# Optimization experiments

Hardware: AMD Instinct MI355X
Metric: run time of the kernel (lower is better)

Reference implementation:

```python
import jax, jax.numpy as jnp
import numpy as np

NUM_LAYERS = 4
HIDDEN = 512
HEADS = 8
DK = HIDDEN // HEADS
REPR_IN = 53
REPR_HID = 32
LN_EPS = 1e-5


def _mask_by_1dmask(x, mask):
    # x: [B,H,L,L], mask: [B,L] bool
    pair = mask[:, :, None] & mask[:, None, :]          # [B,L,L]
    masked = jnp.where(pair[:, None, :, :], x, -jnp.inf)
    all_inf = jnp.all(masked == -jnp.inf, axis=-1, keepdims=True)
    return jnp.where(all_inf, 0.0, masked)


def _layernorm(x, g, b):
    mu = jnp.mean(x, axis=-1, keepdims=True)
    var = jnp.mean((x - mu) ** 2, axis=-1, keepdims=True)
    return (x - mu) * jax.lax.rsqrt(var + LN_EPS) * g + b


def _attn_block(x, mask, refCov, Wq, bq, Wk, bk, Wv, bv, Wo, bo,
                Wr1, br1, Wr2, br2, ln_g, ln_b):
    B, L, h = x.shape
    residual = x
    q = (x @ Wq + bq).reshape(B, L, HEADS, DK).transpose(0, 2, 1, 3)  # [B,H,L,dk]
    k = (x @ Wk + bk).reshape(B, L, HEADS, DK).transpose(0, 2, 1, 3)
    v = (x @ Wv + bv).reshape(B, L, HEADS, DK).transpose(0, 2, 1, 3)
    scores = jnp.einsum('bhid,bhjd->bhij', q, k) / np.sqrt(DK).astype(np.float32)
    scores = _mask_by_1dmask(scores, mask)
    attn_w = jax.nn.softmax(scores, axis=-1)
    # per-pair MLP bias: [B,L,L,53] -> [B,L,L,H] -> [B,H,L,L]
    ref = jax.nn.relu(refCov @ Wr1 + br1) @ Wr2 + br2
    ref = ref.transpose(0, 3, 1, 2)
    ref = _mask_by_1dmask(ref, mask)
    ref_w = jax.nn.softmax(ref, axis=-1)
    comb = attn_w + ref_w
    comb = comb / jnp.sum(comb, axis=-1, keepdims=True)
    out = jnp.einsum('bhij,bhjd->bhid', comb, v)
    out = out.transpose(0, 2, 1, 3).reshape(B, L, h)
    out = out @ Wo + bo
    return _layernorm(residual + out, ln_g, ln_b)


def setup_inputs() -> dict:
    key = jax.random.key(0)
    ks = jax.random.split(key, 20)
    B, L = 8, 384
    s = 0.02
    inp = {
        'x': jax.random.normal(ks[0], (B, L, HIDDEN), jnp.float32),
        'mask': jax.random.randint(ks[1], (B, L), 0, 2) > 0,
        'refCov': jax.random.normal(ks[2], (B, L, L, REPR_IN), jnp.float32),
        'Wq': jax.random.normal(ks[3], (NUM_LAYERS, HIDDEN, HIDDEN)) * s,
        'bq': jnp.zeros((NUM_LAYERS, HIDDEN)),
        'Wk': jax.random.normal(ks[4], (NUM_LAYERS, HIDDEN, HIDDEN)) * s,
        'bk': jnp.zeros((NUM_LAYERS, HIDDEN)),
        'Wv': jax.random.normal(ks[5], (NUM_LAYERS, HIDDEN, HIDDEN)) * s,
        'bv': jnp.zeros((NUM_LAYERS, HIDDEN)),
        'Wo': jax.random.normal(ks[6], (NUM_LAYERS, HIDDEN, HIDDEN)) * s,
        'bo': jnp.zeros((NUM_LAYERS, HIDDEN)),
        'Wr1': jax.random.normal(ks[7], (NUM_LAYERS, REPR_IN, REPR_HID)) * 0.1,
        'br1': jnp.zeros((NUM_LAYERS, REPR_HID)),
        'Wr2': jax.random.normal(ks[8], (NUM_LAYERS, REPR_HID, HEADS)) * 0.1,
        'br2': jnp.zeros((NUM_LAYERS, HEADS)),
        'ln_g': jnp.ones((NUM_LAYERS, HIDDEN)),
        'ln_b': jnp.zeros((NUM_LAYERS, HIDDEN)),
        'fn_g': jnp.ones((HIDDEN,)),
        'fn_b': jnp.zeros((HIDDEN,)),
    }
    return inp


def reference(x, mask, refCov, Wq, bq, Wk, bk, Wv, bv, Wo, bo,
              Wr1, br1, Wr2, br2, ln_g, ln_b, fn_g, fn_b):
    # process_node_feature packs flat nodes into [B,L,h] with zeros at padding;
    # equivalent here to zeroing padded positions of x.
    h = x * mask[:, :, None].astype(x.dtype)
    for i in range(NUM_LAYERS):
        h = _attn_block(h, mask, refCov, Wq[i], bq[i], Wk[i], bk[i],
                        Wv[i], bv[i], Wo[i], bo[i], Wr1[i], br1[i],
                        Wr2[i], br2[i], ln_g[i], ln_b[i])
    h = _layernorm(h, fn_g, fn_b)
    return jnp.sum(h * mask[:, :, None].astype(h.dtype), axis=1)  # [B, HIDDEN]
```

## Files before the change

kernel.cpp:

```cpp
#include <hip/hip_runtime.h>
#include <hip/hip_bf16.h>
#include <cstdint>

constexpr int LSEQ  = 384;
constexpr int BATCH = 8;
constexpr int HID   = 512;
constexpr int NHEAD = 8;
constexpr int DKH   = 64;
constexpr int NLAY  = 4;
constexpr int BL    = BATCH * LSEQ;
constexpr int LL2   = LSEQ * LSEQ;
constexpr int BH    = BATCH * NHEAD;

typedef __bf16 bf16x8 __attribute__((ext_vector_type(8)));
typedef float  f32x4  __attribute__((ext_vector_type(4)));
typedef unsigned short ushort_t;

__device__ inline bf16x8 load_frag(const void* p) {
    uint4 u = *reinterpret_cast<const uint4*>(p);
    return __builtin_bit_cast(bf16x8, u);
}
__device__ inline bf16x8 zero_frag() {
    uint4 u = {0u, 0u, 0u, 0u};
    return __builtin_bit_cast(bf16x8, u);
}
__device__ inline f32x4 mfma16(bf16x8 a, bf16x8 b, f32x4 c) {
    return __builtin_amdgcn_mfma_f32_16x16x32_bf16(a, b, c, 0, 0, 0);
}
__device__ inline float b2f(__hip_bfloat16 v) { return __bfloat162float(v); }
__device__ inline ushort_t bfbits(float f) {
    __hip_bfloat16 b = __float2bfloat16(f);
    return *(ushort_t*)&b;
}

__global__ __launch_bounds__(1024) void mask_norm_kernel(
    const unsigned char* __restrict__ raw, unsigned char* __restrict__ m)
{
    __shared__ int fl;
    const int tid = threadIdx.x;
    if (tid == 0) fl = 0;
    __syncthreads();
    int f = 0;
    for (int i = tid; i < BL; i += 1024) {
        const unsigned char v = raw[i];
        if (v > 1) f |= 1;
        if (v && (i & 3)) f |= 2;
        if (v && ((i & 7) == 4)) f |= 4;
        if (v && ((i & 3) <= 1)) f |= 8;
    }
    if (f) atomicOr(&fl, f);
    __syncthreads();
    const int ff = fl;
    int stride, off;
    if (ff & 1) { if (ff & 8) { stride = 2; off = 0; } else { stride = 4; off = 2; } }
    else if (ff & 2) { stride = 1; off = 0; }
    else if (ff & 4) { stride = 4; off = 0; }
    else             { stride = 8; off = 0; }
    for (int i = tid; i < BL; i += 1024)
        m[i] = raw[(size_t)i * stride + off] ? 1 : 0;
}

__global__ __launch_bounds__(256) void wconv_kernel(
    const float* __restrict__ Wq, const float* __restrict__ Wk,
    const float* __restrict__ Wv, const float* __restrict__ Wo,
    ushort_t* __restrict__ WTqkv, ushort_t* __restrict__ WTo)
{
    __shared__ float tile[32][33];
    const int t = blockIdx.x;
    const int ml = t >> 8;
    const int rest = t & 255;
    const int mi = ml >> 2, l = ml & 3;
    const int tk = (rest & 15) * 32;
    const int tn = (rest >> 4) * 32;
    const float* W = (mi == 0) ? Wq : (mi == 1) ? Wk : (mi == 2) ? Wv : Wo;
    const float* src = W + (size_t)l * HID * HID;
    const int c = threadIdx.x & 31, r = threadIdx.x >> 5;
    for (int rr = r; rr < 32; rr += 8)
        tile[rr][c] = src[(size_t)(tk + rr) * HID + tn + c];
    __syncthreads();
    ushort_t* dst = (mi < 3)
        ? WTqkv + ((size_t)l * 1536 + mi * 512) * HID
        : WTo   + (size_t)l * HID * HID;
    for (int rr = r; rr < 32; rr += 8)
        dst[(size_t)(tn + rr) * HID + tk + c] = bfbits(tile[c][rr]);
}

__global__ __launch_bounds__(256) void refw_kernel(
    const float* __restrict__ Wr1, const float* __restrict__ Wr2,
    ushort_t* __restrict__ W1T, ushort_t* __restrict__ W2T)
{
    const int tid = blockIdx.x * 256 + threadIdx.x;
    if (tid < 4 * 32 * 64) {
        const int l = tid >> 11, rem = tid & 2047;
        const int n = rem >> 6, k = rem & 63;
        W1T[tid] = (k < 53) ? bfbits(Wr1[(l * 53 + k) * 32 + n]) : (ushort_t)0;
    } else if (tid < 4 * 32 * 64 + 4 * 16 * 32) {
        const int t2 = tid - 8192;
        const int l = t2 >> 9, rem = t2 & 511;
        const int n = rem >> 5, k = rem & 31;
        W2T[t2] = (n < 8) ? bfbits(Wr2[(l * 32 + k) * 8 + n]) : (ushort_t)0;
    }
}

__global__ __launch_bounds__(256) void pack_kernel(
    const float* __restrict__ x, const unsigned char* __restrict__ mask,
    float* __restrict__ h, __hip_bfloat16* __restrict__ hb)
{
    const int idx = blockIdx.x * 256 + threadIdx.x;
    const int row = idx >> 9;
    const float v = mask[row] ? x[idx] : 0.f;
    h[idx] = v;
    hb[idx] = __float2bfloat16(v);
}

__global__ __launch_bounds__(256) void refmlp_kernel(
    const float* __restrict__ refCov,
    const ushort_t* __restrict__ W1T, const float* __restrict__ br1,
    const ushort_t* __restrict__ W2T, const float* __restrict__ br2,
    __hip_bfloat16* __restrict__ refL)
{
    __shared__ ushort_t smem[256 * 56];

    const int tid = threadIdx.x;
    const int w = tid >> 6, lane = tid & 63;
    const int lr = lane & 15, quad = lane >> 4;
    const size_t p0 = (size_t)blockIdx.x * 256;
    const int b = (int)(p0 / LL2);
    const int rem0 = (int)(p0 - (size_t)b * LL2);

    const float4* src4 = reinterpret_cast<const float4*>(refCov + p0 * 53);
    for (int f = tid; f < 3392; f += 256) {
        float4 v = src4[f];
        const int e = f * 4;
        #pragma unroll
        for (int k = 0; k < 4; ++k) {
            const int g = e + k;
            const int row = g / 53;
            const int col = g - row * 53;
            smem[row * 56 + col] = bfbits(((const float*)&v)[k]);
        }
    }
    smem[tid * 56 + 53] = 0;
    smem[tid * 56 + 54] = 0;
    smem[tid * 56 + 55] = 0;
    __syncthreads();

    bf16x8 afr[4][2];
    #pragma unroll
    for (int mi = 0; mi < 4; ++mi) {
        const ushort_t* rp = smem + (w * 64 + mi * 16 + lr) * 56;
        afr[mi][0] = load_frag(rp + quad * 8);
        afr[mi][1] = (quad < 3) ? load_frag(rp + 32 + quad * 8) : zero_frag();
    }
    __syncthreads();

    ushort_t* C1w = smem + w * 2560;

    #pragma unroll
    for (int l = 0; l < NLAY; ++l) {
        const float bias0 = br1[l * 32 + lr];
        const float bias1 = br1[l * 32 + 16 + lr];
        const float bias2 = br2[l * 8 + (lr & 7)];
        bf16x8 w1f[2][2];
        #pragma unroll
        for (int ni = 0; ni < 2; ++ni)
            #pragma unroll
            for (int ks = 0; ks < 2; ++ks)
                w1f[ni][ks] = load_frag(W1T + ((l * 32 + ni * 16 + lr) * 64) + ks * 32 + quad * 8);
        bf16x8 w2f = load_frag(W2T + (l * 16 + lr) * 32 + quad * 8);

        f32x4 acc[4][2];
        #pragma unroll
        for (int mi = 0; mi < 4; ++mi) {
            acc[mi][0] = (f32x4){bias0, bias0, bias0, bias0};
            acc[mi][1] = (f32x4){bias1, bias1, bias1, bias1};
        }
        #pragma unroll
        for (int mi = 0; mi < 4; ++mi) {
            acc[mi][0] = mfma16(afr[mi][0], w1f[0][0], acc[mi][0]);
            acc[mi][0] = mfma16(afr[mi][1], w1f[0][1], acc[mi][0]);
            acc[mi][1] = mfma16(afr[mi][0], w1f[1][0], acc[mi][1]);
            acc[mi][1] = mfma16(afr[mi][1], w1f[1][1], acc[mi][1]);
        }
        #pragma unroll
        for (int mi = 0; mi < 4; ++mi)
            #pragma unroll
            for (int ni = 0; ni < 2; ++ni)
                #pragma unroll
                for (int r = 0; r < 4; ++r)
                    C1w[(mi * 16 + quad * 4 + r) * 40 + ni * 16 + lr] =
                        bfbits(fmaxf(acc[mi][ni][r], 0.f));

        #pragma unroll
        for (int mi = 0; mi < 4; ++mi) {
            bf16x8 a2 = load_frag(C1w + (mi * 16 + lr) * 40 + quad * 8);
            f32x4 a = (f32x4){bias2, bias2, bias2, bias2};
            a = mfma16(a2, w2f, a);
            if (lr < 8) {
                uint2 pk;
                pk.x = (unsigned)bfbits(a[0]) | ((unsigned)bfbits(a[1]) << 16);
                pk.y = (unsigned)bfbits(a[2]) | ((unsigned)bfbits(a[3]) << 16);
                const size_t plane = ((size_t)(l * 8 + b) * 8 + lr) * LL2;
                *reinterpret_cast<uint2*>((ushort_t*)refL + plane + rem0 +
                                          w * 64 + mi * 16 + quad * 4) = pk;
            }
        }
    }
}

__global__ __launch_bounds__(256) void gemm_qkv_kernel(
    const __hip_bfloat16* __restrict__ A,
    const __hip_bfloat16* __restrict__ BT,
    const float* __restrict__ bq, const float* __restrict__ bk,
    const float* __restrict__ bv,
    __hip_bfloat16* __restrict__ q, __hip_bfloat16* __restrict__ kk,
    __hip_bfloat16* __restrict__ vT)
{
    const int bm = blockIdx.x % (BL / 64);
    const int bn = blockIdx.x / (BL / 64);
    const int wv = threadIdx.x >> 6;
    const int lane = threadIdx.x & 63;
    const int lr = lane & 15, quad = lane >> 4;
    const int m0 = bm * 64 + (wv & 1) * 32;
    const int n0g = bn * 64 + (wv >> 1) * 32;
    f32x4 acc[2][2];
    #pragma unroll
    for (int i = 0; i < 2; ++i)
        #pragma unroll
        for (int j = 0; j < 2; ++j) acc[i][j] = (f32x4){0.f, 0.f, 0.f, 0.f};
    const __hip_bfloat16* a0p = A + (size_t)(m0 + lr) * HID;
    const __hip_bfloat16* a1p = A + (size_t)(m0 + 16 + lr) * HID;
    const __hip_bfloat16* b0p = BT + (size_t)(n0g + lr) * HID;
    const __hip_bfloat16* b1p = BT + (size_t)(n0g + 16 + lr) * HID;
    #pragma unroll 4
    for (int k0 = 0; k0 < HID; k0 += 32) {
        const int ka = k0 + quad * 8;
        bf16x8 a0 = load_frag(a0p + ka);
        bf16x8 a1 = load_frag(a1p + ka);
        bf16x8 b0 = load_frag(b0p + ka);
        bf16x8 b1 = load_frag(b1p + ka);
        acc[0][0] = mfma16(a0, b0, acc[0][0]);
        acc[0][1] = mfma16(a0, b1, acc[0][1]);
        acc[1][0] = mfma16(a1, b0, acc[1][0]);
        acc[1][1] = mfma16(a1, b1, acc[1][1]);
    }
    const int mat = n0g >> 9;
    const float* bias = (mat == 0) ? bq : (mat == 1) ? bk : bv;
    const float scale = (mat == 0) ? 0.125f : 1.0f;
    __hip_bfloat16* outp = (mat == 0) ? q : (mat == 1) ? kk : vT;
    #pragma unroll
    for (int mi = 0; mi < 2; ++mi)
        #pragma unroll
        for (int ni = 0; ni < 2; ++ni)
            #pragma unroll
            for (int r = 0; r < 4; ++r) {
                const int m = m0 + mi * 16 + quad * 4 + r;
                const int ng = n0g + ni * 16 + lr;
                const int n = ng & 511;
                float v = (acc[mi][ni][r] + bias[n]) * scale;
                const int bb = m / LSEQ, ii = m % LSEQ;
                const int hh = n >> 6, d = n & 63;
                if (mat == 2)
                    outp[((size_t)(bb * NHEAD + hh) * DKH + d) * LSEQ + ii] = __float2bfloat16(v);
                else
                    outp[((size_t)(bb * NHEAD + hh) * LSEQ + ii) * DKH + d] = __float2bfloat16(v);
            }
}

__global__ __launch_bounds__(256) void gemm_oproj_kernel(
    const __hip_bfloat16* __restrict__ A,
    const __hip_bfloat16* __restrict__ BT,
    const float* __restrict__ bias,
    float* __restrict__ outf)
{
    const int bm = blockIdx.x % (BL / 64);
    const int bn = blockIdx.x / (BL / 64);
    const int wv = threadIdx.x >> 6;
    const int lane = threadIdx.x & 63;
    const int lr = lane & 15, quad = lane >> 4;
    const int m0 = bm * 64 + (wv & 1) * 32;
    const int n0 = bn * 64 + (wv >> 1) * 32;
    f32x4 acc[2][2];
    #pragma unroll
    for (int i = 0; i < 2; ++i)
        #pragma unroll
        for (int j = 0; j < 2; ++j) acc[i][j] = (f32x4){0.f, 0.f, 0.f, 0.f};
    const __hip_bfloat16* a0p = A + (size_t)(m0 + lr) * HID;
    const __hip_bfloat16* a1p = A + (size_t)(m0 + 16 + lr) * HID;
    const __hip_bfloat16* b0p = BT + (size_t)(n0 + lr) * HID;
    const __hip_bfloat16* b1p = BT + (size_t)(n0 + 16 + lr) * HID;
    #pragma unroll 4
    for (int k0 = 0; k0 < HID; k0 += 32) {
        const int ka = k0 + quad * 8;
        bf16x8 a0 = load_frag(a0p + ka);
        bf16x8 a1 = load_frag(a1p + ka);
        bf16x8 b0 = load_frag(b0p + ka);
        bf16x8 b1 = load_frag(b1p + ka);
        acc[0][0] = mfma16(a0, b0, acc[0][0]);
        acc[0][1] = mfma16(a0, b1, acc[0][1]);
        acc[1][0] = mfma16(a1, b0, acc[1][0]);
        acc[1][1] = mfma16(a1, b1, acc[1][1]);
    }
    #pragma unroll
    for (int mi = 0; mi < 2; ++mi)
        #pragma unroll
        for (int ni = 0; ni < 2; ++ni)
            #pragma unroll
            for (int r = 0; r < 4; ++r) {
                const int m = m0 + mi * 16 + quad * 4 + r;
                const int n = n0 + ni * 16 + lr;
                outf[(size_t)m * HID + n] = acc[mi][ni][r] + bias[n];
            }
}

__global__ __launch_bounds__(256) void attn_fused_kernel(
    const __hip_bfloat16* __restrict__ Q,
    const __hip_bfloat16* __restrict__ Km,
    const __hip_bfloat16* __restrict__ VT,
    const __hip_bfloat16* __restrict__ refl,
    const unsigned char* __restrict__ mask,
    __hip_bfloat16* __restrict__ AO)
{
    __shared__ __align__(16) ushort_t Pl[32 * 392];
    __shared__ float redm_s[2][2][16], redm_r[2][2][16];
    __shared__ float reds_s[2][2][16], reds_r[2][2][16];

    const int bh = blockIdx.x / 12;
    const int i0 = (blockIdx.x % 12) * 32;
    const int b  = bh >> 3, hh = bh & 7;
    const int w = threadIdx.x >> 6, lane = threadIdx.x & 63;
    const int s = w & 1, h2 = w >> 1;
    const int lr = lane & 15, quad = lane >> 4;

    const __hip_bfloat16* qb = Q  + (size_t)bh * LSEQ * DKH;
    const __hip_bfloat16* kb = Km + (size_t)bh * LSEQ * DKH;
    const unsigned char* mrow = mask + b * LSEQ;

    f32x4 acc[12];
    #pragma unroll
    for (int nt = 0; nt < 12; ++nt) acc[nt] = (f32x4){0.f, 0.f, 0.f, 0.f};
    #pragma unroll
    for (int k0 = 0; k0 < DKH; k0 += 32) {
        const int ka = k0 + quad * 8;
        bf16x8 a = load_frag(qb + (size_t)(i0 + s * 16 + lr) * DKH + ka);
        #pragma unroll
        for (int nt = 0; nt < 12; ++nt) {
            bf16x8 bf = load_frag(kb + (size_t)(h2 * 192 + nt * 16 + lr) * DKH + ka);
            acc[nt] = mfma16(a, bf, acc[nt]);
        }
    }

    bool vm[12];
    #pragma unroll
    for (int nt = 0; nt < 12; ++nt)
        vm[nt] = mrow[h2 * 192 + nt * 16 + lr] != 0;

    const __hip_bfloat16* rbase = refl + (size_t)bh * LL2 +
                                  (size_t)(i0 + s * 16) * LSEQ + h2 * 192;
    float rv[12][4];
    #pragma unroll
    for (int nt = 0; nt < 12; ++nt)
        #pragma unroll
        for (int r = 0; r < 4; ++r)
            rv[nt][r] = b2f(rbase[(size_t)(quad * 4 + r) * LSEQ + nt * 16 + lr]);

    float ms[4], mr2[4];
    #pragma unroll
    for (int r = 0; r < 4; ++r) { ms[r] = -1e30f; mr2[r] = -1e30f; }
    #pragma unroll
    for (int nt = 0; nt < 12; ++nt)
        #pragma unroll
        for (int r = 0; r < 4; ++r) {
            acc[nt][r] = vm[nt] ? acc[nt][r] : -1e30f;
            rv[nt][r]  = vm[nt] ? rv[nt][r]  : -1e30f;
            ms[r]  = fmaxf(ms[r],  acc[nt][r]);
            mr2[r] = fmaxf(mr2[r], rv[nt][r]);
        }
    #pragma unroll
    for (int off = 8; off > 0; off >>= 1)
        #pragma unroll
        for (int r = 0; r < 4; ++r) {
            ms[r]  = fmaxf(ms[r],  __shfl_xor(ms[r],  off));
            mr2[r] = fmaxf(mr2[r], __shfl_xor(mr2[r], off));
        }
    if (lr == 0)
        #pragma unroll
        for (int r = 0; r < 4; ++r) {
            redm_s[s][h2][quad * 4 + r] = ms[r];
            redm_r[s][h2][quad * 4 + r] = mr2[r];
        }
    __syncthreads();
    #pragma unroll
    for (int r = 0; r < 4; ++r) {
        ms[r]  = fmaxf(redm_s[s][0][quad * 4 + r], redm_s[s][1][quad * 4 + r]);
        mr2[r] = fmaxf(redm_r[s][0][quad * 4 + r], redm_r[s][1][quad * 4 + r]);
    }

    float Ss[4] = {0.f, 0.f, 0.f, 0.f}, Sr[4] = {0.f, 0.f, 0.f, 0.f};
    #pragma unroll
    for (int nt = 0; nt < 12; ++nt)
        #pragma unroll
        for (int r = 0; r < 4; ++r) {
            acc[nt][r] = __expf(acc[nt][r] - ms[r]);  Ss[r] += acc[nt][r];
            rv[nt][r]  = __expf(rv[nt][r]  - mr2[r]); Sr[r] += rv[nt][r];
        }
    #pragma unroll
    for (int off = 8; off > 0; off >>= 1)
        #pragma unroll
        for (int r = 0; r < 4; ++r) {
            Ss[r] += __shfl_xor(Ss[r], off);
            Sr[r] += __shfl_xor(Sr[r], off);
        }
    if (lr == 0)
        #pragma unroll
        for (int r = 0; r < 4; ++r) {
            reds_s[s][h2][quad * 4 + r] = Ss[r];
            reds_r[s][h2][quad * 4 + r] = Sr[r];
        }
    __syncthreads();

    float cs[4], cr[4], rm[4];
    #pragma unroll
    for (int r = 0; r < 4; ++r) {
        const float SsF = reds_s[s][0][quad * 4 + r] + reds_s[s][1][quad * 4 + r];
        const float SrF = reds_r[s][0][quad * 4 + r] + reds_r[s][1][quad * 4 + r];
        cs[r] = 0.5f / SsF;
        cr[r] = 0.5f / SrF;
        rm[r] = mrow[i0 + s * 16 + quad * 4 + r] ? 1.f : 0.f;
    }
    #pragma unroll
    for (int nt = 0; nt < 12; ++nt)
        #pragma unroll
        for (int r = 0; r < 4; ++r)
            Pl[(s * 16 + quad * 4 + r) * 392 + h2 * 192 + nt * 16 + lr] =
                bfbits((acc[nt][r] * cs[r] + rv[nt][r] * cr[r]) * rm[r]);
    __syncthreads();

    const __hip_bfloat16* vb = VT + (size_t)bh * DKH * LSEQ;
    f32x4 oa[2];
    oa[0] = (f32x4){0.f, 0.f, 0.f, 0.f};
    oa[1] = (f32x4){0.f, 0.f, 0.f, 0.f};
    #pragma unroll 4
    for (int k0 = 0; k0 < LSEQ; k0 += 32) {
        const int ka = k0 + quad * 8;
        bf16x8 a = load_frag(Pl + (s * 16 + lr) * 392 + ka);
        #pragma unroll
        for (int dt = 0; dt < 2; ++dt) {
            bf16x8 bf = load_frag(vb + (size_t)(h2 * 32 + dt * 16 + lr) * LSEQ + ka);
            oa[dt] = mfma16(a, bf, oa[dt]);
        }
    }
    #pragma unroll
    for (int dt = 0; dt < 2; ++dt)
        #pragma unroll
        for (int r = 0; r < 4; ++r)
            AO[(size_t)(b * LSEQ + i0 + s * 16 + quad * 4 + r) * HID +
               hh * DKH + h2 * 32 + dt * 16 + lr] = __float2bfloat16(oa[dt][r]);
}

__global__ __launch_bounds__(256) void ln_kernel(
    const float* __restrict__ resid, const float* __restrict__ proj,
    const float* __restrict__ g, const float* __restrict__ beta,
    float* __restrict__ outf, __hip_bfloat16* __restrict__ outb,
    const unsigned char* __restrict__ mask, int flags)
{
    const int row = blockIdx.x, tid = threadIdx.x;
    const size_t base = (size_t)row * HID;
    float x0 = resid[base + tid], x1 = resid[base + tid + 256];
    if (flags & 1) { x0 += proj[base + tid]; x1 += proj[base + tid + 256]; }
    float s = x0 + x1, s2 = x0 * x0 + x1 * x1;
    #pragma unroll
    for (int off = 32; off > 0; off >>= 1) {
        s += __shfl_xor(s, off);
        s2 += __shfl_xor(s2, off);
    }
    __shared__ float rs[4], rs2[4];
    if ((tid & 63) == 0) { rs[tid >> 6] = s; rs2[tid >> 6] = s2; }
    __syncthreads();
    s = rs[0] + rs[1] + rs[2] + rs[3];
    s2 = rs2[0] + rs2[1] + rs2[2] + rs2[3];
    const float mu = s * (1.f / HID);
    const float var = s2 * (1.f / HID) - mu * mu;
    const float rstd = rsqrtf(var + 1e-5f);
    float y0 = (x0 - mu) * rstd * g[tid] + beta[tid];
    float y1 = (x1 - mu) * rstd * g[tid + 256] + beta[tid + 256];
    if ((flags & 2) && !mask[row]) { y0 = 0.f; y1 = 0.f; }
    outf[base + tid] = y0;
    outf[base + tid + 256] = y1;
    if (flags & 4) {
        outb[base + tid] = __float2bfloat16(y0);
        outb[base + tid + 256] = __float2bfloat16(y1);
    }
}

__global__ __launch_bounds__(512) void reduce_kernel(
    const float* __restrict__ hf, float* __restrict__ out)
{
    const int b = blockIdx.x, c = threadIdx.x;
    float s = 0.f;
    for (int i = 0; i < LSEQ; ++i)
        s += hf[((size_t)(b * LSEQ + i)) * HID + c];
    out[b * HID + c] = s;
}

extern "C" void kernel_launch(void* const* d_in, const int* in_sizes, int n_in,
                              void* d_out, int out_size, void* d_ws, size_t ws_size,
                              hipStream_t stream)
{
    const float* x   = (const float*)d_in[0];
    const unsigned char* mraw = (const unsigned char*)d_in[1];
    const float* refCov = (const float*)d_in[2];
    const float* Wq = (const float*)d_in[3];
    const float* bq = (const float*)d_in[4];
    const float* Wk = (const float*)d_in[5];
    const float* bk = (const float*)d_in[6];
    const float* Wv = (const float*)d_in[7];
    const float* bv = (const float*)d_in[8];
    const float* Wo = (const float*)d_in[9];
    const float* bo = (const float*)d_in[10];
    const float* Wr1 = (const float*)d_in[11];
    const float* br1 = (const float*)d_in[12];
    const float* Wr2 = (const float*)d_in[13];
    const float* br2 = (const float*)d_in[14];
    const float* ln_g = (const float*)d_in[15];
    const float* ln_b = (const float*)d_in[16];
    const float* fn_g = (const float*)d_in[17];
    const float* fn_b = (const float*)d_in[18];
    float* outp = (float*)d_out;

    char* ws = (char*)d_ws;
    size_t off = 0;
    auto alloc = [&](size_t bytes) -> char* {
        char* p = ws + off;
        off += (bytes + 255) & ~(size_t)255;
        return p;
    };
    __hip_bfloat16* refL  = (__hip_bfloat16*)alloc((size_t)NLAY * BH * LL2 * 2);
    float*          h     = (float*)alloc((size_t)BL * HID * 4);
    __hip_bfloat16* hb    = (__hip_bfloat16*)alloc((size_t)BL * HID * 2);
    __hip_bfloat16* q     = (__hip_bfloat16*)alloc((size_t)BH * LSEQ * DKH * 2);
    __hip_bfloat16* kk    = (__hip_bfloat16*)alloc((size_t)BH * LSEQ * DKH * 2);
    __hip_bfloat16* vT    = (__hip_bfloat16*)alloc((size_t)BH * DKH * LSEQ * 2);
    float*          S     = (float*)alloc((size_t)BH * LL2 * 4);
    __hip_bfloat16* AO    = (__hip_bfloat16*)alloc((size_t)BL * HID * 2);
    float*          proj  = (float*)alloc((size_t)BL * HID * 4);
    ushort_t*       WTqkv = (ushort_t*)alloc((size_t)NLAY * 1536 * HID * 2);
    ushort_t*       WTo   = (ushort_t*)alloc((size_t)NLAY * HID * HID * 2);
    ushort_t*       W1T   = (ushort_t*)alloc((size_t)4 * 32 * 64 * 2);
    ushort_t*       W2T   = (ushort_t*)alloc((size_t)4 * 16 * 32 * 2);
    unsigned char*  msk   = (unsigned char*)alloc(BL);
    float*          hfin  = S;

    mask_norm_kernel<<<1, 1024, 0, stream>>>(mraw, msk);
    wconv_kernel<<<4096, 256, 0, stream>>>(Wq, Wk, Wv, Wo, WTqkv, WTo);
    refw_kernel<<<40, 256, 0, stream>>>(Wr1, Wr2, W1T, W2T);
    pack_kernel<<<6144, 256, 0, stream>>>(x, msk, h, hb);
    refmlp_kernel<<<4608, 256, 0, stream>>>(refCov, W1T, br1, W2T, br2, refL);

    for (int l = 0; l < NLAY; ++l) {
        const __hip_bfloat16* WTl = (const __hip_bfloat16*)(WTqkv + (size_t)l * 1536 * HID);
        const __hip_bfloat16* WTol = (const __hip_bfloat16*)(WTo + (size_t)l * HID * HID);
        gemm_qkv_kernel<<<1152, 256, 0, stream>>>(hb, WTl, bq + l * HID, bk + l * HID,
                                                  bv + l * HID, q, kk, vT);
        attn_fused_kernel<<<768, 256, 0, stream>>>(q, kk, vT,
                                                   refL + (size_t)l * BH * LL2, msk, AO);
        gemm_oproj_kernel<<<384, 256, 0, stream>>>(AO, WTol, bo + l * HID, proj);
        ln_kernel<<<3072, 256, 0, stream>>>(h, proj, ln_g + l * HID, ln_b + l * HID,
                                            h, hb, nullptr, 1 | 4);
    }
    ln_kernel<<<3072, 256, 0, stream>>>(h, nullptr, fn_g, fn_b, hfin, nullptr, msk, 2);
    reduce_kernel<<<8, 512, 0, stream>>>(hfin, outp);
}
```

Baseline: 840.2 us.

## Merge setup kernels, widen attention to 512 threads, warp-per-row layernorm with atomic final reduce

Merges the weight-conversion kernels into one launch and the pack step into the refCov MLP launch, cutting launch count. The fused attention kernel moves to 8 waves per block, each covering 96 key columns and 16 output dims, which halves per-wave register pressure and raises parallelism. LayerNorm now uses one wave per row with float4 loads and no shared-memory reduction. The final LN+masked sum becomes a single kernel that skips masked rows and accumulates with atomicAdd into an output zeroed in the mask kernel; this adds atomic contention and makes summation order nondeterministic.

```diff
diff --git a/kernel.cpp b/kernel.cpp
--- a/kernel.cpp
+++ b/kernel.cpp
@@ -34,7 +34,8 @@
 }
 
 __global__ __launch_bounds__(1024) void mask_norm_kernel(
-    const unsigned char* __restrict__ raw, unsigned char* __restrict__ m)
+    const unsigned char* __restrict__ raw, unsigned char* __restrict__ m,
+    float* __restrict__ outz)
 {
     __shared__ int fl;
     const int tid = threadIdx.x;
@@ -49,6 +50,7 @@
         if (v && ((i & 3) <= 1)) f |= 8;
     }
     if (f) atomicOr(&fl, f);
+    for (int i = tid; i < BATCH * HID; i += 1024) outz[i] = 0.f;
     __syncthreads();
     const int ff = fl;
     int stride, off;
@@ -60,66 +62,65 @@
         m[i] = raw[(size_t)i * stride + off] ? 1 : 0;
 }
 
-__global__ __launch_bounds__(256) void wconv_kernel(
+__global__ __launch_bounds__(256) void wconv_refw_kernel(
     const float* __restrict__ Wq, const float* __restrict__ Wk,
     const float* __restrict__ Wv, const float* __restrict__ Wo,
-    ushort_t* __restrict__ WTqkv, ushort_t* __restrict__ WTo)
-{
-    __shared__ float tile[32][33];
-    const int t = blockIdx.x;
-    const int ml = t >> 8;
-    const int rest = t & 255;
-    const int mi = ml >> 2, l = ml & 3;
-    const int tk = (rest & 15) * 32;
-    const int tn = (rest >> 4) * 32;
-    const float* W = (mi == 0) ? Wq : (mi == 1) ? Wk : (mi == 2) ? Wv : Wo;
-    const float* src = W + (size_t)l * HID * HID;
-    const int c = threadIdx.x & 31, r = threadIdx.x >> 5;
-    for (int rr = r; rr < 32; rr += 8)
-        tile[rr][c] = src[(size_t)(tk + rr) * HID + tn + c];
-    __syncthreads();
-    ushort_t* dst = (mi < 3)
-        ? WTqkv + ((size_t)l * 1536 + mi * 512) * HID
-        : WTo   + (size_t)l * HID * HID;
-    for (int rr = r; rr < 32; rr += 8)
-        dst[(size_t)(tn + rr) * HID + tk + c] = bfbits(tile[c][rr]);
-}
-
-__global__ __launch_bounds__(256) void refw_kernel(
+    ushort_t* __restrict__ WTqkv, ushort_t* __restrict__ WTo,
     const float* __restrict__ Wr1, const float* __restrict__ Wr2,
     ushort_t* __restrict__ W1T, ushort_t* __restrict__ W2T)
 {
-    const int tid = blockIdx.x * 256 + threadIdx.x;
-    if (tid < 4 * 32 * 64) {
-        const int l = tid >> 11, rem = tid & 2047;
-        const int n = rem >> 6, k = rem & 63;
-        W1T[tid] = (k < 53) ? bfbits(Wr1[(l * 53 + k) * 32 + n]) : (ushort_t)0;
-    } else if (tid < 4 * 32 * 64 + 4 * 16 * 32) {
-        const int t2 = tid - 8192;
-        const int l = t2 >> 9, rem = t2 & 511;
-        const int n = rem >> 5, k = rem & 31;
-        W2T[t2] = (n < 8) ? bfbits(Wr2[(l * 32 + k) * 8 + n]) : (ushort_t)0;
-    }
-}
-
-__global__ __launch_bounds__(256) void pack_kernel(
-    const float* __restrict__ x, const unsigned char* __restrict__ mask,
-    float* __restrict__ h, __hip_bfloat16* __restrict__ hb)
-{
-    const int idx = blockIdx.x * 256 + threadIdx.x;
-    const int row = idx >> 9;
-    const float v = mask[row] ? x[idx] : 0.f;
-    h[idx] = v;
-    hb[idx] = __float2bfloat16(v);
-}
-
-__global__ __launch_bounds__(256) void refmlp_kernel(
+    __shared__ float tile[32][33];
+    if (blockIdx.x < 4096) {
+        const int t = blockIdx.x;
+        const int ml = t >> 8;
+        const int rest = t & 255;
+        const int mi = ml >> 2, l = ml & 3;
+        const int tk = (rest & 15) * 32;
+        const int tn = (rest >> 4) * 32;
+        const float* W = (mi == 0) ? Wq : (mi == 1) ? Wk : (mi == 2) ? Wv : Wo;
+        const float* src = W + (size_t)l * HID * HID;
+        const int c = threadIdx.x & 31, r = threadIdx.x >> 5;
+        for (int rr = r; rr < 32; rr += 8)
+            tile[rr][c] = src[(size_t)(tk + rr) * HID + tn + c];
+        __syncthreads();
+        ushort_t* dst = (mi < 3)
+            ? WTqkv + ((size_t)l * 1536 + mi * 512) * HID
+            : WTo   + (size_t)l * HID * HID;
+        for (int rr = r; rr < 32; rr += 8)
+            dst[(size_t)(tn + rr) * HID + tk + c] = bfbits(tile[c][rr]);
+    } else {
+        const int tid = (blockIdx.x - 4096) * 256 + threadIdx.x;
+        if (tid < 4 * 32 * 64) {
+            const int l = tid >> 11, rem = tid & 2047;
+            const int n = rem >> 6, k = rem & 63;
+            W1T[tid] = (k < 53) ? bfbits(Wr1[(l * 53 + k) * 32 + n]) : (ushort_t)0;
+        } else if (tid < 4 * 32 * 64 + 4 * 16 * 32) {
+            const int t2 = tid - 8192;
+            const int l = t2 >> 9, rem = t2 & 511;
+            const int n = rem >> 5, k = rem & 31;
+            W2T[t2] = (n < 8) ? bfbits(Wr2[(l * 32 + k) * 8 + n]) : (ushort_t)0;
+        }
+    }
+}
+
+__global__ __launch_bounds__(256) void refmlp_pack_kernel(
     const float* __restrict__ refCov,
     const ushort_t* __restrict__ W1T, const float* __restrict__ br1,
     const ushort_t* __restrict__ W2T, const float* __restrict__ br2,
-    __hip_bfloat16* __restrict__ refL)
+    __hip_bfloat16* __restrict__ refL,
+    const float* __restrict__ x, const unsigned char* __restrict__ mask,
+    float* __restrict__ h, __hip_bfloat16* __restrict__ hb)
 {
     __shared__ ushort_t smem[256 * 56];
+
+    if (blockIdx.x >= 4608) {
+        const int idx = (blockIdx.x - 4608) * 256 + threadIdx.x;
+        const int row = idx >> 9;
+        const float v = mask[row] ? x[idx] : 0.f;
+        h[idx] = v;
+        hb[idx] = __float2bfloat16(v);
+        return;
+    }
 
     const int tid = threadIdx.x;
     const int w = tid >> 6, lane = tid & 63;
@@ -313,7 +314,7 @@
             }
 }
 
-__global__ __launch_bounds__(256) void attn_fused_kernel(
+__global__ __launch_bounds__(512) void attn_fused_kernel(
     const __hip_bfloat16* __restrict__ Q,
     const __hip_bfloat16* __restrict__ Km,
     const __hip_bfloat16* __restrict__ VT,
@@ -322,44 +323,44 @@
     __hip_bfloat16* __restrict__ AO)
 {
     __shared__ __align__(16) ushort_t Pl[32 * 392];
-    __shared__ float redm_s[2][2][16], redm_r[2][2][16];
-    __shared__ float reds_s[2][2][16], reds_r[2][2][16];
+    __shared__ float redm_s[2][4][16], redm_r[2][4][16];
+    __shared__ float reds_s[2][4][16], reds_r[2][4][16];
 
     const int bh = blockIdx.x / 12;
     const int i0 = (blockIdx.x % 12) * 32;
     const int b  = bh >> 3, hh = bh & 7;
     const int w = threadIdx.x >> 6, lane = threadIdx.x & 63;
-    const int s = w & 1, h2 = w >> 1;
+    const int s = w & 1, h4 = w >> 1;
     const int lr = lane & 15, quad = lane >> 4;
 
     const __hip_bfloat16* qb = Q  + (size_t)bh * LSEQ * DKH;
     const __hip_bfloat16* kb = Km + (size_t)bh * LSEQ * DKH;
     const unsigned char* mrow = mask + b * LSEQ;
 
-    f32x4 acc[12];
-    #pragma unroll
-    for (int nt = 0; nt < 12; ++nt) acc[nt] = (f32x4){0.f, 0.f, 0.f, 0.f};
+    f32x4 acc[6];
+    #pragma unroll
+    for (int nt = 0; nt < 6; ++nt) acc[nt] = (f32x4){0.f, 0.f, 0.f, 0.f};
     #pragma unroll
     for (int k0 = 0; k0 < DKH; k0 += 32) {
         const int ka = k0 + quad * 8;
         bf16x8 a = load_frag(qb + (size_t)(i0 + s * 16 + lr) * DKH + ka);
         #pragma unroll
-        for (int nt = 0; nt < 12; ++nt) {
-            bf16x8 bf = load_frag(kb + (size_t)(h2 * 192 + nt * 16 + lr) * DKH + ka);
+        for (int nt = 0; nt < 6; ++nt) {
+            bf16x8 bf = load_frag(kb + (size_t)(h4 * 96 + nt * 16 + lr) * DKH + ka);
             acc[nt] = mfma16(a, bf, acc[nt]);
         }
     }
 
-    bool vm[12];
-    #pragma unroll
-    for (int nt = 0; nt < 12; ++nt)
-        vm[nt] = mrow[h2 * 192 + nt * 16 + lr] != 0;
+    bool vm[6];
+    #pragma unroll
+    for (int nt = 0; nt < 6; ++nt)
+        vm[nt] = mrow[h4 * 96 + nt * 16 + lr] != 0;
 
     const __hip_bfloat16* rbase = refl + (size_t)bh * LL2 +
-                                  (size_t)(i0 + s * 16) * LSEQ + h2 * 192;
-    float rv[12][4];
-    #pragma unroll
-    for (int nt = 0; nt < 12; ++nt)
+                                  (size_t)(i0 + s * 16) * LSEQ + h4 * 96;
+    float rv[6][4];
+    #pragma unroll
+    for (int nt = 0; nt < 6; ++nt)
         #pragma unroll
         for (int r = 0; r < 4; ++r)
             rv[nt][r] = b2f(rbase[(size_t)(quad * 4 + r) * LSEQ + nt * 16 + lr]);
@@ -368,7 +369,7 @@
     #pragma unroll
     for (int r = 0; r < 4; ++r) { ms[r] = -1e30f; mr2[r] = -1e30f; }
     #pragma unroll
-    for (int nt = 0; nt < 12; ++nt)
+    for (int nt = 0; nt < 6; ++nt)
         #pragma unroll
         for (int r = 0; r < 4; ++r) {
             acc[nt][r] = vm[nt] ? acc[nt][r] : -1e30f;
@@ -386,19 +387,22 @@
     if (lr == 0)
         #pragma unroll
         for (int r = 0; r < 4; ++r) {
-            redm_s[s][h2][quad * 4 + r] = ms[r];
-            redm_r[s][h2][quad * 4 + r] = mr2[r];
+            redm_s[s][h4][quad * 4 + r] = ms[r];
+            redm_r[s][h4][quad * 4 + r] = mr2[r];
         }
     __syncthreads();
     #pragma unroll
     for (int r = 0; r < 4; ++r) {
-        ms[r]  = fmaxf(redm_s[s][0][quad * 4 + r], redm_s[s][1][quad * 4 + r]);
-        mr2[r] = fmaxf(redm_r[s][0][quad * 4 + r], redm_r[s][1][quad * 4 + r]);
+        const int x = quad * 4 + r;
+        ms[r]  = fmaxf(fmaxf(redm_s[s][0][x], redm_s[s][1][x]),
+                       fmaxf(redm_s[s][2][x], redm_s[s][3][x]));
+        mr2[r] = fmaxf(fmaxf(redm_r[s][0][x], redm_r[s][1][x]),
+                       fmaxf(redm_r[s][2][x], redm_r[s][3][x]));
     }
 
     float Ss[4] = {0.f, 0.f, 0.f, 0.f}, Sr[4] = {0.f, 0.f, 0.f, 0.f};
     #pragma unroll
-    for (int nt = 0; nt < 12; ++nt)
+    for (int nt = 0; nt < 6; ++nt)
         #pragma unroll
         for (int r = 0; r < 4; ++r) {
             acc[nt][r] = __expf(acc[nt][r] - ms[r]);  Ss[r] += acc[nt][r];
@@ -414,93 +418,126 @@
     if (lr == 0)
         #pragma unroll
         for (int r = 0; r < 4; ++r) {
-            reds_s[s][h2][quad * 4 + r] = Ss[r];
-            reds_r[s][h2][quad * 4 + r] = Sr[r];
+            reds_s[s][h4][quad * 4 + r] = Ss[r];
+            reds_r[s][h4][quad * 4 + r] = Sr[r];
         }
     __syncthreads();
 
     float cs[4], cr[4], rm[4];
     #pragma unroll
     for (int r = 0; r < 4; ++r) {
-        const float SsF = reds_s[s][0][quad * 4 + r] + reds_s[s][1][quad * 4 + r];
-        const float SrF = reds_r[s][0][quad * 4 + r] + reds_r[s][1][quad * 4 + r];
+        const int x = quad * 4 + r;
+        const float SsF = reds_s[s][0][x] + reds_s[s][1][x] +
+                          reds_s[s][2][x] + reds_s[s][3][x];
+        const float SrF = reds_r[s][0][x] + reds_r[s][1][x] +
+                          reds_r[s][2][x] + reds_r[s][3][x];
         cs[r] = 0.5f / SsF;
         cr[r] = 0.5f / SrF;
-        rm[r] = mrow[i0 + s * 16 + quad * 4 + r] ? 1.f : 0.f;
-    }
-    #pragma unroll
-    for (int nt = 0; nt < 12; ++nt)
+        rm[r] = mrow[i0 + s * 16 + x] ? 1.f : 0.f;
+    }
+    #pragma unroll
+    for (int nt = 0; nt < 6; ++nt)
         #pragma unroll
         for (int r = 0; r < 4; ++r)
-            Pl[(s * 16 + quad * 4 + r) * 392 + h2 * 192 + nt * 16 + lr] =
+            Pl[(s * 16 + quad * 4 + r) * 392 + h4 * 96 + nt * 16 + lr] =
                 bfbits((acc[nt][r] * cs[r] + rv[nt][r] * cr[r]) * rm[r]);
     __syncthreads();
 
     const __hip_bfloat16* vb = VT + (size_t)bh * DKH * LSEQ;
-    f32x4 oa[2];
-    oa[0] = (f32x4){0.f, 0.f, 0.f, 0.f};
-    oa[1] = (f32x4){0.f, 0.f, 0.f, 0.f};
+    f32x4 oa = (f32x4){0.f, 0.f, 0.f, 0.f};
     #pragma unroll 4
     for (int k0 = 0; k0 < LSEQ; k0 += 32) {
         const int ka = k0 + quad * 8;
         bf16x8 a = load_frag(Pl + (s * 16 + lr) * 392 + ka);
-        #pragma unroll
-        for (int dt = 0; dt < 2; ++dt) {
-            bf16x8 bf = load_frag(vb + (size_t)(h2 * 32 + dt * 16 + lr) * LSEQ + ka);
-            oa[dt] = mfma16(a, bf, oa[dt]);
-        }
-    }
-    #pragma unroll
-    for (int dt = 0; dt < 2; ++dt)
-        #pragma unroll
-        for (int r = 0; r < 4; ++r)
-            AO[(size_t)(b * LSEQ + i0 + s * 16 + quad * 4 + r) * HID +
-               hh * DKH + h2 * 32 + dt * 16 + lr] = __float2bfloat16(oa[dt][r]);
-}
-
-__global__ __launch_bounds__(256) void ln_kernel(
+        bf16x8 bf = load_frag(vb + (size_t)(h4 * 16 + lr) * LSEQ + ka);
+        oa = mfma16(a, bf, oa);
+    }
+    #pragma unroll
+    for (int r = 0; r < 4; ++r)
+        AO[(size_t)(b * LSEQ + i0 + s * 16 + quad * 4 + r) * HID +
+           hh * DKH + h4 * 16 + lr] = __float2bfloat16(oa[r]);
+}
+
+__global__ __launch_bounds__(256) void ln4_kernel(
     const float* __restrict__ resid, const float* __restrict__ proj,
     const float* __restrict__ g, const float* __restrict__ beta,
-    float* __restrict__ outf, __hip_bfloat16* __restrict__ outb,
-    const unsigned char* __restrict__ mask, int flags)
-{
-    const int row = blockIdx.x, tid = threadIdx.x;
-    const size_t base = (size_t)row * HID;
-    float x0 = resid[base + tid], x1 = resid[base + tid + 256];
-    if (flags & 1) { x0 += proj[base + tid]; x1 += proj[base + tid + 256]; }
-    float s = x0 + x1, s2 = x0 * x0 + x1 * x1;
+    float* __restrict__ outf, __hip_bfloat16* __restrict__ outb)
+{
+    const int w = threadIdx.x >> 6, lane = threadIdx.x & 63;
+    const int row = blockIdx.x * 4 + w;
+    const size_t base = (size_t)row * HID + lane * 8;
+    float4 a0 = *reinterpret_cast<const float4*>(resid + base);
+    float4 a1 = *reinterpret_cast<const float4*>(resid + base + 4);
+    const float4 p0 = *reinterpret_cast<const float4*>(proj + base);
+    const float4 p1 = *reinterpret_cast<const float4*>(proj + base + 4);
+    a0.x += p0.x; a0.y += p0.y; a0.z += p0.z; a0.w += p0.w;
+    a1.x += p1.x; a1.y += p1.y; a1.z += p1.z; a1.w += p1.w;
+    float xs[8] = {a0.x, a0.y, a0.z, a0.w, a1.x, a1.y, a1.z, a1.w};
+    float sum = 0.f, sq = 0.f;
+    #pragma unroll
+    for (int j = 0; j < 8; ++j) { sum += xs[j]; sq += xs[j] * xs[j]; }
     #pragma unroll
     for (int off = 32; off > 0; off >>= 1) {
-        s += __shfl_xor(s, off);
-        s2 += __shfl_xor(s2, off);
-    }
-    __shared__ float rs[4], rs2[4];
-    if ((tid & 63) == 0) { rs[tid >> 6] = s; rs2[tid >> 6] = s2; }
-    __syncthreads();
-    s = rs[0] + rs[1] + rs[2] + rs[3];
-    s2 = rs2[0] + rs2[1] + rs2[2] + rs2[3];
-    const float mu = s * (1.f / HID);
-    const float var = s2 * (1.f / HID) - mu * mu;
+        sum += __shfl_xor(sum, off);
+        sq  += __shfl_xor(sq, off);
+    }
+    const float mu = sum * (1.f / HID);
+    const float var = sq * (1.f / HID) - mu * mu;
     const float rstd = rsqrtf(var + 1e-5f);
-    float y0 = (x0 - mu) * rstd * g[tid] + beta[tid];
-    float y1 = (x1 - mu) * rstd * g[tid + 256] + beta[tid + 256];
-    if ((flags & 2) && !mask[row]) { y0 = 0.f; y1 = 0.f; }
-    outf[base + tid] = y0;
-    outf[base + tid + 256] = y1;
-    if (flags & 4) {
-        outb[base + tid] = __float2bfloat16(y0);
-        outb[base + tid + 256] = __float2bfloat16(y1);
-    }
-}
-
-__global__ __launch_bounds__(512) void reduce_kernel(
-    const float* __restrict__ hf, float* __restrict__ out)
-{
-    const int b = blockIdx.x, c = threadIdx.x;
-    float s = 0.f;
-    for (int i = 0; i < LSEQ; ++i)
-        s += hf[((size_t)(b * LSEQ + i)) * HID + c];
-    out[b * HID + c] = s;
+    const float4 g0 = *reinterpret_cast<const float4*>(g + lane * 8);
+    const float4 g1 = *reinterpret_cast<const float4*>(g + lane * 8 + 4);
+    const float4 b0 = *reinterpret_cast<const float4*>(beta + lane * 8);
+    const float4 b1 = *reinterpret_cast<const float4*>(beta + lane * 8 + 4);
+    const float gg[8] = {g0.x, g0.y, g0.z, g0.w, g1.x, g1.y, g1.z, g1.w};
+    const float bb[8] = {b0.x, b0.y, b0.z, b0.w, b1.x, b1.y, b1.z, b1.w};
+    float y[8];
+    #pragma unroll
+    for (int j = 0; j < 8; ++j) y[j] = (xs[j] - mu) * rstd * gg[j] + bb[j];
+    float4 o0 = {y[0], y[1], y[2], y[3]}, o1 = {y[4], y[5], y[6], y[7]};
+    *reinterpret_cast<float4*>(outf + base) = o0;
+    *reinterpret_cast<float4*>(outf + base + 4) = o1;
+    uint4 pb;
+    pb.x = (unsigned)bfbits(y[0]) | ((unsigned)bfbits(y[1]) << 16);
+    pb.y = (unsigned)bfbits(y[2]) | ((unsigned)bfbits(y[3]) << 16);
+    pb.z = (unsigned)bfbits(y[4]) | ((unsigned)bfbits(y[5]) << 16);
+    pb.w = (unsigned)bfbits(y[6]) | ((unsigned)bfbits(y[7]) << 16);
+    *reinterpret_cast<uint4*>(outb + base) = pb;
+}
+
+__global__ __launch_bounds__(256) void ln_final_kernel(
+    const float* __restrict__ resid, const float* __restrict__ g,
+    const float* __restrict__ beta, const unsigned char* __restrict__ mask,
+    float* __restrict__ out)
+{
+    const int w = threadIdx.x >> 6, lane = threadIdx.x & 63;
+    const int row = blockIdx.x * 4 + w;
+    if (!mask[row]) return;
+    const int b = row / LSEQ;
+    const size_t base = (size_t)row * HID + lane * 8;
+    const float4 a0 = *reinterpret_cast<const float4*>(resid + base);
+    const float4 a1 = *reinterpret_cast<const float4*>(resid + base + 4);
+    float xs[8] = {a0.x, a0.y, a0.z, a0.w, a1.x, a1.y, a1.z, a1.w};
+    float sum = 0.f, sq = 0.f;
+    #pragma unroll
+    for (int j = 0; j < 8; ++j) { sum += xs[j]; sq += xs[j] * xs[j]; }
+    #pragma unroll
+    for (int off = 32; off > 0; off >>= 1) {
+        sum += __shfl_xor(sum, off);
+        sq  += __shfl_xor(sq, off);
+    }
+    const float mu = sum * (1.f / HID);
+    const float var = sq * (1.f / HID) - mu * mu;
+    const float rstd = rsqrtf(var + 1e-5f);
+    const float4 g0 = *reinterpret_cast<const float4*>(g + lane * 8);
+    const float4 g1 = *reinterpret_cast<const float4*>(g + lane * 8 + 4);
+    const float4 b0 = *reinterpret_cast<const float4*>(beta + lane * 8);
+    const float4 b1 = *reinterpret_cast<const float4*>(beta + lane * 8 + 4);
+    const float gg[8] = {g0.x, g0.y, g0.z, g0.w, g1.x, g1.y, g1.z, g1.w};
+    const float bb[8] = {b0.x, b0.y, b0.z, b0.w, b1.x, b1.y, b1.z, b1.w};
+    float* orow = out + (size_t)b * HID + lane * 8;
+    #pragma unroll
+    for (int j = 0; j < 8; ++j)
+        atomicAdd(orow + j, (xs[j] - mu) * rstd * gg[j] + bb[j]);
 }
 
 extern "C" void kernel_launch(void* const* d_in, const int* in_sizes, int n_in,
@@ -541,7 +578,6 @@
     __hip_bfloat16* q     = (__hip_bfloat16*)alloc((size_t)BH * LSEQ * DKH * 2);
     __hip_bfloat16* kk    = (__hip_bfloat16*)alloc((size_t)BH * LSEQ * DKH * 2);
     __hip_bfloat16* vT    = (__hip_bfloat16*)alloc((size_t)BH * DKH * LSEQ * 2);
-    float*          S     = (float*)alloc((size_t)BH * LL2 * 4);
     __hip_bfloat16* AO    = (__hip_bfloat16*)alloc((size_t)BL * HID * 2);
     float*          proj  = (float*)alloc((size_t)BL * HID * 4);
     ushort_t*       WTqkv = (ushort_t*)alloc((size_t)NLAY * 1536 * HID * 2);
@@ -549,25 +585,23 @@
     ushort_t*       W1T   = (ushort_t*)alloc((size_t)4 * 32 * 64 * 2);
     ushort_t*       W2T   = (ushort_t*)alloc((size_t)4 * 16 * 32 * 2);
     unsigned char*  msk   = (unsigned char*)alloc(BL);
-    float*          hfin  = S;
-
-    mask_norm_kernel<<<1, 1024, 0, stream>>>(mraw, msk);
-    wconv_kernel<<<4096, 256, 0, stream>>>(Wq, Wk, Wv, Wo, WTqkv, WTo);
-    refw_kernel<<<40, 256, 0, stream>>>(Wr1, Wr2, W1T, W2T);
-    pack_kernel<<<6144, 256, 0, stream>>>(x, msk, h, hb);
-    refmlp_kernel<<<4608, 256, 0, stream>>>(refCov, W1T, br1, W2T, br2, refL);
+
+    mask_norm_kernel<<<1, 1024, 0, stream>>>(mraw, msk, outp);
+    wconv_refw_kernel<<<4136, 256, 0, stream>>>(Wq, Wk, Wv, Wo, WTqkv, WTo,
+                                                Wr1, Wr2, W1T, W2T);
+    refmlp_pack_kernel<<<10752, 256, 0, stream>>>(refCov, W1T, br1, W2T, br2, refL,
+                                                  x, msk, h, hb);
 
     for (int l = 0; l < NLAY; ++l) {
         const __hip_bfloat16* WTl = (const __hip_bfloat16*)(WTqkv + (size_t)l * 1536 * HID);
         const __hip_bfloat16* WTol = (const __hip_bfloat16*)(WTo + (size_t)l * HID * HID);
         gemm_qkv_kernel<<<1152, 256, 0, stream>>>(hb, WTl, bq + l * HID, bk + l * HID,
                                                   bv + l * HID, q, kk, vT);
-        attn_fused_kernel<<<768, 256, 0, stream>>>(q, kk, vT,
+        attn_fused_kernel<<<768, 512, 0, stream>>>(q, kk, vT,
                                                    refL + (size_t)l * BH * LL2, msk, AO);
         gemm_oproj_kernel<<<384, 256, 0, stream>>>(AO, WTol, bo + l * HID, proj);
-        ln_kernel<<<3072, 256, 0, stream>>>(h, proj, ln_g + l * HID, ln_b + l * HID,
-                                            h, hb, nullptr, 1 | 4);
-    }
-    ln_kernel<<<3072, 256, 0, stream>>>(h, nullptr, fn_g, fn_b, hfin, nullptr, msk, 2);
-    reduce_kernel<<<8, 512, 0, stream>>>(hfin, outp);
-}
+        ln4_kernel<<<768, 256, 0, stream>>>(h, proj, ln_g + l * HID, ln_b + l * HID,
+                                            h, hb);
+    }
+    ln_final_kernel<<<768, 256, 0, stream>>>(h, fn_g, fn_b, msk, outp);
+}
```

Measured after the change: 858.7 us. 1.02x slower.
